# Performance work log

Measured on AMD Instinct MI355X. Metric: run time of the kernel, lower is better.

The kernel has to match this reference:

```python
import jax, jax.numpy as jnp
import numpy as np

N = 8192
IN_FEATS = 512
OUT_FEATS = 256
NEG_SLOPE = 0.01  # torch nn.LeakyReLU default


def setup_inputs() -> dict:
    key = jax.random.key(0)
    k_adj, k_feat, k_w, k_b, k_a1, k_a2 = jax.random.split(key, 6)
    adj_matrix = jax.random.uniform(k_adj, (N, N), dtype=jnp.float32)
    eye_matrix = jnp.eye(N, dtype=jnp.float32)  # identity adjacency, per AAGNN usage
    subgraph_feats = jax.random.normal(k_feat, (N, IN_FEATS), dtype=jnp.float32)
    node_mask = jnp.ones((N,), dtype=bool)
    # nn.Linear(in_feats, out_feats) params (kaiming-uniform-ish init scale)
    lim = 1.0 / np.sqrt(IN_FEATS)
    W = jax.random.uniform(k_w, (OUT_FEATS, IN_FEATS), minval=-lim, maxval=lim, dtype=jnp.float32)
    b = jax.random.uniform(k_b, (OUT_FEATS,), minval=-lim, maxval=lim, dtype=jnp.float32)
    # a_1, a_2 ~ torch.rand(1, out_feats)
    a_1 = jax.random.uniform(k_a1, (1, OUT_FEATS), dtype=jnp.float32)
    a_2 = jax.random.uniform(k_a2, (1, OUT_FEATS), dtype=jnp.float32)
    return {"adj_matrix": adj_matrix, "eye_matrix": eye_matrix,
            "subgraph_feats": subgraph_feats, "node_mask": node_mask,
            "W": W, "b": b, "a_1": a_1, "a_2": a_2}


def reference(adj_matrix, eye_matrix, subgraph_feats, node_mask, W, b, a_1, a_2):
    # z = Linear(subgraph_feats)  -> [N, out]
    z = subgraph_feats @ W.T + b
    zi = jnp.sum(a_1 * z, axis=1, keepdims=True)  # [N,1]
    zj = jnp.sum(a_2 * z, axis=1, keepdims=True)  # [N,1]
    # masked attention scores: adj*zi + adj*(eye*zj), leakyrelu, row softmax
    scores = jax.nn.leaky_relu(adj_matrix * zi + adj_matrix * (eye_matrix * zj),
                               negative_slope=NEG_SLOPE)
    att = jax.nn.softmax(scores, axis=1)  # [N,N]
    h = z - att @ z  # [N, out]
    out = jax.nn.relu(h)
    # original returns relu(h[node_mask]); mask is all-True -> same rows, static shape
    return jnp.where(node_mask[:, None], out, 0.0)
```

## Files before the change

### kernel.cpp

```cpp
#include <hip/hip_runtime.h>

#define N_NODES 8192
#define IN_F 512
#define OUT_F 256
#define KSPLIT 4
#define KCHUNK (N_NODES / KSPLIT)

typedef float f32x4 __attribute__((ext_vector_type(4)));
typedef short short8 __attribute__((ext_vector_type(8)));
typedef short short4v __attribute__((ext_vector_type(4)));

__device__ __forceinline__ unsigned short f2bf(float f) {
  unsigned int u = __float_as_uint(f);
  return (unsigned short)((u + 0x8000u) >> 16);
}

__device__ __forceinline__ short8 pack8(const float4& a, const float4& b) {
  short8 r;
  r[0] = (short)f2bf(a.x); r[1] = (short)f2bf(a.y);
  r[2] = (short)f2bf(a.z); r[3] = (short)f2bf(a.w);
  r[4] = (short)f2bf(b.x); r[5] = (short)f2bf(b.y);
  r[6] = (short)f2bf(b.z); r[7] = (short)f2bf(b.w);
  return r;
}

__global__ __launch_bounds__(256) void zgemm_mfma(
    const float* __restrict__ feats, const float* __restrict__ W,
    const float* __restrict__ bias, float* __restrict__ z,
    unsigned short* __restrict__ zT) {
  const int tid = threadIdx.x;
  const int w = tid >> 6;
  const int l = tid & 63;
  const int l4 = l >> 4;
  const int lm = l & 15;
  const int ib = blockIdx.x * 32;

  f32x4 acc[2][4];
#pragma unroll
  for (int a = 0; a < 2; ++a)
#pragma unroll
    for (int b = 0; b < 4; ++b) acc[a][b] = (f32x4){0.f, 0.f, 0.f, 0.f};

#pragma unroll 2
  for (int ks = 0; ks < 16; ++ks) {
    const int k0 = ks * 32 + l4 * 8;
    short8 afr[2], bfr[4];
#pragma unroll
    for (int it = 0; it < 2; ++it) {
      const float* p = &feats[(size_t)(ib + it * 16 + lm) * IN_F + k0];
      afr[it] = pack8(*(const float4*)p, *(const float4*)(p + 4));
    }
#pragma unroll
    for (int nt = 0; nt < 4; ++nt) {
      const float* p = &W[(size_t)(w * 64 + nt * 16 + lm) * IN_F + k0];
      bfr[nt] = pack8(*(const float4*)p, *(const float4*)(p + 4));
    }
#pragma unroll
    for (int it = 0; it < 2; ++it)
#pragma unroll
      for (int nt = 0; nt < 4; ++nt)
        acc[it][nt] = __builtin_amdgcn_mfma_f32_16x16x32_bf16(
            afr[it], bfr[nt], acc[it][nt], 0, 0, 0);
  }

#pragma unroll
  for (int nt = 0; nt < 4; ++nt) {
    const int col = w * 64 + nt * 16 + lm;
    const float bv = bias[col];
#pragma unroll
    for (int it = 0; it < 2; ++it)
#pragma unroll
      for (int r = 0; r < 4; ++r) {
        const int row = ib + it * 16 + l4 * 4 + r;
        const float v = acc[it][nt][r] + bv;
        z[(size_t)row * OUT_F + col] = v;
        zT[(size_t)col * N_NODES + row] = f2bf(v);
      }
  }
}

__global__ void zizj_kernel(const float* __restrict__ z,
                            const float* __restrict__ a1v,
                            const float* __restrict__ a2v,
                            float* __restrict__ zi, float* __restrict__ zj) {
  const int w = threadIdx.x >> 6;
  const int l = threadIdx.x & 63;
  const int row = blockIdx.x * 4 + w;
  const float4 zv = *(const float4*)&z[(size_t)row * OUT_F + l * 4];
  const float4 A1 = *(const float4*)&a1v[l * 4];
  const float4 A2 = *(const float4*)&a2v[l * 4];
  float si = zv.x * A1.x + zv.y * A1.y + zv.z * A1.z + zv.w * A1.w;
  float sj = zv.x * A2.x + zv.y * A2.y + zv.z * A2.z + zv.w * A2.w;
#pragma unroll
  for (int off = 32; off > 0; off >>= 1) {
    si += __shfl_xor(si, off);
    sj += __shfl_xor(sj, off);
  }
  if (l == 0) {
    zi[row] = si;
    zj[row] = sj;
  }
}

__global__ __launch_bounds__(256) void p_kernel(
    const float* __restrict__ adj, const float* __restrict__ zi_in,
    const float* __restrict__ zj_in, unsigned short* __restrict__ Pn) {
  __shared__ float red[4];
  const int row = blockIdx.x;
  const int tid = threadIdx.x;
  const float zir = zi_in[row];
  const float zjr = zj_in[row];
  const float* rp = adj + (size_t)row * N_NODES + tid * 4;

  f32x4 a[8];
#pragma unroll
  for (int c = 0; c < 8; ++c)
    a[c] = __builtin_nontemporal_load((const f32x4*)(rp + c * 1024));

  float psum = 0.f;
#pragma unroll
  for (int c = 0; c < 8; ++c)
#pragma unroll
    for (int e = 0; e < 4; ++e) {
      const int j = c * 1024 + tid * 4 + e;
      const float av = a[c][e];
      float s = av * zir;
      if (j == row) s += av * zjr;
      s = fmaxf(s, 0.01f * s);
      psum += __expf(s);
    }
#pragma unroll
  for (int off = 32; off > 0; off >>= 1) psum += __shfl_xor(psum, off);
  if ((tid & 63) == 0) red[tid >> 6] = psum;
  __syncthreads();
  const float rinv = 1.f / (red[0] + red[1] + red[2] + red[3]);

  unsigned short* op = Pn + (size_t)row * N_NODES + tid * 4;
#pragma unroll
  for (int c = 0; c < 8; ++c) {
    short4v v;
#pragma unroll
    for (int e = 0; e < 4; ++e) {
      const int j = c * 1024 + tid * 4 + e;
      const float av = a[c][e];
      float s = av * zir;
      if (j == row) s += av * zjr;
      s = fmaxf(s, 0.01f * s);
      v[e] = (short)f2bf(__expf(s) * rinv);
    }
    *(short4v*)(op + c * 1024) = v;
  }
}

__global__ __launch_bounds__(256) void pz_gemm(
    const unsigned short* __restrict__ Pn,
    const unsigned short* __restrict__ zT, float* __restrict__ acc_ws) {
  __shared__ __align__(16) unsigned short Pt[2][64][64];
  __shared__ __align__(16) unsigned short Zt[2][256][64];
  const int tid = threadIdx.x;
  const int w = tid >> 6;
  const int l = tid & 63;
  const int l4 = l >> 4;
  const int lm = l & 15;
  const int mt = blockIdx.x & 127;
  const int kc = blockIdx.x >> 7;
  const int ib = mt * 64;
  const int jb0 = kc * KCHUNK;

  f32x4 acc[4][4];
#pragma unroll
  for (int a = 0; a < 4; ++a)
#pragma unroll
    for (int b = 0; b < 4; ++b) acc[a][b] = (f32x4){0.f, 0.f, 0.f, 0.f};

  const int NST = KCHUNK / 64;

  {
    const int jb = jb0;
#pragma unroll
    for (int m = 0; m < 2; ++m) {
      const int g = m * 256 + tid, r = g >> 3, s = g & 7;
      *(short8*)&Pt[0][r][(s ^ (r & 7)) * 8] =
          *(const short8*)&Pn[(size_t)(ib + r) * N_NODES + jb + s * 8];
    }
#pragma unroll
    for (int m = 0; m < 8; ++m) {
      const int g = m * 256 + tid, r = g >> 3, s = g & 7;
      *(short8*)&Zt[0][r][(s ^ (r & 7)) * 8] =
          *(const short8*)&zT[(size_t)r * N_NODES + jb + s * 8];
    }
  }

  for (int st = 0; st < NST; ++st) {
    const int b = st & 1;
    __syncthreads();

    short8 pg[2], zg[8];
    if (st + 1 < NST) {
      const int jb = jb0 + (st + 1) * 64;
#pragma unroll
      for (int m = 0; m < 2; ++m) {
        const int g = m * 256 + tid, r = g >> 3, s = g & 7;
        pg[m] = *(const short8*)&Pn[(size_t)(ib + r) * N_NODES + jb + s * 8];
      }
#pragma unroll
      for (int m = 0; m < 8; ++m) {
        const int g = m * 256 + tid, r = g >> 3, s = g & 7;
        zg[m] = *(const short8*)&zT[(size_t)r * N_NODES + jb + s * 8];
      }
    }

    short8 afr[4][2], bfr[2][4];
#pragma unroll
    for (int it = 0; it < 4; ++it) {
      const int r = it * 16 + lm;
#pragma unroll
      for (int kk = 0; kk < 2; ++kk)
        afr[it][kk] = *(const short8*)&Pt[b][r][((kk * 4 + l4) ^ (r & 7)) * 8];
    }
#pragma unroll
    for (int nt = 0; nt < 4; ++nt) {
      const int r = w * 64 + nt * 16 + lm;
#pragma unroll
      for (int kk = 0; kk < 2; ++kk)
        bfr[kk][nt] = *(const short8*)&Zt[b][r][((kk * 4 + l4) ^ (r & 7)) * 8];
    }
#pragma unroll
    for (int it = 0; it < 4; ++it)
#pragma unroll
      for (int kk = 0; kk < 2; ++kk)
#pragma unroll
        for (int nt = 0; nt < 4; ++nt)
          acc[it][nt] = __builtin_amdgcn_mfma_f32_16x16x32_bf16(
              afr[it][kk], bfr[kk][nt], acc[it][nt], 0, 0, 0);

    __syncthreads();

    if (st + 1 < NST) {
#pragma unroll
      for (int m = 0; m < 2; ++m) {
        const int g = m * 256 + tid, r = g >> 3, s = g & 7;
        *(short8*)&Pt[b ^ 1][r][(s ^ (r & 7)) * 8] = pg[m];
      }
#pragma unroll
      for (int m = 0; m < 8; ++m) {
        const int g = m * 256 + tid, r = g >> 3, s = g & 7;
        *(short8*)&Zt[b ^ 1][r][(s ^ (r & 7)) * 8] = zg[m];
      }
    }
  }

#pragma unroll
  for (int it = 0; it < 4; ++it)
#pragma unroll
    for (int nt = 0; nt < 4; ++nt)
#pragma unroll
      for (int r = 0; r < 4; ++r) {
        const int gi = ib + it * 16 + l4 * 4 + r;
        const int gn = w * 64 + nt * 16 + lm;
        acc_ws[((size_t)kc * N_NODES + gi) * OUT_F + gn] = acc[it][nt][r];
      }
}

__global__ void finalize_kernel(const float* __restrict__ z,
                                const float* __restrict__ acc_ws,
                                float* __restrict__ out) {
  const int i = blockIdx.x;
  const int n = threadIdx.x;
  float a = 0.f;
#pragma unroll
  for (int kc = 0; kc < KSPLIT; ++kc)
    a += acc_ws[((size_t)kc * N_NODES + i) * OUT_F + n];
  const float v = z[(size_t)i * OUT_F + n] - a;
  out[(size_t)i * OUT_F + n] = fmaxf(v, 0.f);
}

extern "C" void kernel_launch(void* const* d_in, const int* in_sizes, int n_in,
                              void* d_out, int out_size, void* d_ws,
                              size_t ws_size, hipStream_t stream) {
  (void)in_sizes; (void)n_in; (void)out_size; (void)ws_size;
  const float* adj = (const float*)d_in[0];
  const float* feats = (const float*)d_in[2];
  const float* W = (const float*)d_in[4];
  const float* bias = (const float*)d_in[5];
  const float* a1v = (const float*)d_in[6];
  const float* a2v = (const float*)d_in[7];
  float* out = (float*)d_out;

  char* ws = (char*)d_ws;
  float* z = (float*)ws;
  unsigned short* zT = (unsigned short*)(ws + ((size_t)8 << 20));
  float* zi = (float*)(ws + ((size_t)12 << 20));
  float* zj = zi + N_NODES;
  float* acc_ws = (float*)(ws + ((size_t)16 << 20));
  unsigned short* Pn = (unsigned short*)(ws + ((size_t)96 << 20));

  hipLaunchKernelGGL(zgemm_mfma, dim3(N_NODES / 32), dim3(256), 0, stream,
                     feats, W, bias, z, zT);
  hipLaunchKernelGGL(zizj_kernel, dim3(N_NODES / 4), dim3(256), 0, stream, z,
                     a1v, a2v, zi, zj);
  hipLaunchKernelGGL(p_kernel, dim3(N_NODES), dim3(256), 0, stream, adj, zi,
                     zj, Pn);
  hipLaunchKernelGGL(pz_gemm, dim3(128 * KSPLIT), dim3(256), 0, stream, Pn,
                     zT, acc_ws);
  hipLaunchKernelGGL(finalize_kernel, dim3(N_NODES), dim3(256), 0, stream, z,
                     acc_ws, out);
}
```

Measured before the change: 160.4 us.

## Stage pz_gemm tiles with direct global-to-LDS loads and cache exp values

The pz_gemm double-buffer pipeline now uses global_load_lds to copy P and zT tiles straight into shared memory, with the XOR swizzle moved into the per-lane global address. This removes the register staging and the separate LDS write phase, and leaves one barrier per stage. Launch bounds request two blocks per CU. In p_kernel the exp values are kept in registers from the sum pass, so the second pass no longer recomputes leaky-relu and exp. The risks are higher register pressure and whether the async LDS loads are fully complete at the single barrier.

Measured after the change: 162.1 us. Within noise of the previous version (+1.1%).

```diff
diff --git a/kernel.cpp b/kernel.cpp
--- a/kernel.cpp
+++ b/kernel.cpp
@@ -22,6 +22,13 @@
   r[4] = (short)f2bf(b.x); r[5] = (short)f2bf(b.y);
   r[6] = (short)f2bf(b.z); r[7] = (short)f2bf(b.w);
   return r;
+}
+
+__device__ __forceinline__ void gload_lds16(const unsigned short* g,
+                                            unsigned short* l) {
+  __builtin_amdgcn_global_load_lds(
+      (const __attribute__((address_space(1))) unsigned int*)g,
+      (__attribute__((address_space(3))) unsigned int*)l, 16, 0, 0);
 }
 
 __global__ __launch_bounds__(256) void zgemm_mfma(
@@ -117,6 +124,7 @@
   for (int c = 0; c < 8; ++c)
     a[c] = __builtin_nontemporal_load((const f32x4*)(rp + c * 1024));
 
+  float p[32];
   float psum = 0.f;
 #pragma unroll
   for (int c = 0; c < 8; ++c)
@@ -127,8 +135,13 @@
       float s = av * zir;
       if (j == row) s += av * zjr;
       s = fmaxf(s, 0.01f * s);
-      psum += __expf(s);
-    }
+      const float pe = __expf(s);
+      p[c * 4 + e] = pe;
+      psum += pe;
+    }
+#pragma unroll
+  for (int i = 0; i < 32; ++i) asm volatile("" : "+v"(p[i]));
+
 #pragma unroll
   for (int off = 32; off > 0; off >>= 1) psum += __shfl_xor(psum, off);
   if ((tid & 63) == 0) red[tid >> 6] = psum;
@@ -140,19 +153,12 @@
   for (int c = 0; c < 8; ++c) {
     short4v v;
 #pragma unroll
-    for (int e = 0; e < 4; ++e) {
-      const int j = c * 1024 + tid * 4 + e;
-      const float av = a[c][e];
-      float s = av * zir;
-      if (j == row) s += av * zjr;
-      s = fmaxf(s, 0.01f * s);
-      v[e] = (short)f2bf(__expf(s) * rinv);
-    }
+    for (int e = 0; e < 4; ++e) v[e] = (short)f2bf(p[c * 4 + e] * rinv);
     *(short4v*)(op + c * 1024) = v;
   }
 }
 
-__global__ __launch_bounds__(256) void pz_gemm(
+__global__ __launch_bounds__(256, 2) void pz_gemm(
     const unsigned short* __restrict__ Pn,
     const unsigned short* __restrict__ zT, float* __restrict__ acc_ws) {
   __shared__ __align__(16) unsigned short Pt[2][64][64];
@@ -167,6 +173,9 @@
   const int ib = mt * 64;
   const int jb0 = kc * KCHUNK;
 
+  const int rsub = w * 8 + (l >> 3);
+  const int csw = ((l & 7) ^ (l >> 3)) * 8;
+
   f32x4 acc[4][4];
 #pragma unroll
   for (int a = 0; a < 4; ++a)
@@ -175,40 +184,24 @@
 
   const int NST = KCHUNK / 64;
 
-  {
-    const int jb = jb0;
-#pragma unroll
-    for (int m = 0; m < 2; ++m) {
-      const int g = m * 256 + tid, r = g >> 3, s = g & 7;
-      *(short8*)&Pt[0][r][(s ^ (r & 7)) * 8] =
-          *(const short8*)&Pn[(size_t)(ib + r) * N_NODES + jb + s * 8];
-    }
-#pragma unroll
-    for (int m = 0; m < 8; ++m) {
-      const int g = m * 256 + tid, r = g >> 3, s = g & 7;
-      *(short8*)&Zt[0][r][(s ^ (r & 7)) * 8] =
-          *(const short8*)&zT[(size_t)r * N_NODES + jb + s * 8];
-    }
-  }
+#define STAGE(buf, jb)                                                       \
+  {                                                                          \
+    _Pragma("unroll") for (int m = 0; m < 2; ++m) {                          \
+      gload_lds16(&Pn[(size_t)(ib + m * 32 + rsub) * N_NODES + (jb) + csw],  \
+                  &Pt[buf][0][0] + (m * 256 + w * 64) * 8);                  \
+    }                                                                        \
+    _Pragma("unroll") for (int m = 0; m < 8; ++m) {                          \
+      gload_lds16(&zT[(size_t)(m * 32 + rsub) * N_NODES + (jb) + csw],       \
+                  &Zt[buf][0][0] + (m * 256 + w * 64) * 8);                  \
+    }                                                                        \
+  }
+
+  STAGE(0, jb0);
+  __syncthreads();
 
   for (int st = 0; st < NST; ++st) {
     const int b = st & 1;
-    __syncthreads();
-
-    short8 pg[2], zg[8];
-    if (st + 1 < NST) {
-      const int jb = jb0 + (st + 1) * 64;
-#pragma unroll
-      for (int m = 0; m < 2; ++m) {
-        const int g = m * 256 + tid, r = g >> 3, s = g & 7;
-        pg[m] = *(const short8*)&Pn[(size_t)(ib + r) * N_NODES + jb + s * 8];
-      }
-#pragma unroll
-      for (int m = 0; m < 8; ++m) {
-        const int g = m * 256 + tid, r = g >> 3, s = g & 7;
-        zg[m] = *(const short8*)&zT[(size_t)r * N_NODES + jb + s * 8];
-      }
-    }
+    if (st + 1 < NST) STAGE(b ^ 1, jb0 + (st + 1) * 64);
 
     short8 afr[4][2], bfr[2][4];
 #pragma unroll
@@ -235,19 +228,6 @@
               afr[it][kk], bfr[kk][nt], acc[it][nt], 0, 0, 0);
 
     __syncthreads();
-
-    if (st + 1 < NST) {
-#pragma unroll
-      for (int m = 0; m < 2; ++m) {
-        const int g = m * 256 + tid, r = g >> 3, s = g & 7;
-        *(short8*)&Pt[b ^ 1][r][(s ^ (r & 7)) * 8] = pg[m];
-      }
-#pragma unroll
-      for (int m = 0; m < 8; ++m) {
-        const int g = m * 256 + tid, r = g >> 3, s = g & 7;
-        *(short8*)&Zt[b ^ 1][r][(s ^ (r & 7)) * 8] = zg[m];
-      }
-    }
   }
 
 #pragma unroll
```

## Load z operand directly from global, cache exp values, raise K-split

Applied to the files above, without the earlier changes.

The PZ GEMM stops staging the z tile in shared memory and has each wave read its MFMA B fragments straight from global memory, relying on L2 since all row blocks share zT. This cuts LDS use so more blocks can be resident, with a launch-bounds occupancy hint of 3. The K-split rises from 4 to 8 for more parallelism, at the cost of a larger partial-sum workspace that the finalize step must reduce. The softmax kernel keeps the 32 exponentials in registers instead of recomputing them in the second pass, which trades more registers for fewer exp evaluations.

After: 190.1 us. +18.6%, slower.

```diff
diff --git a/kernel.cpp b/kernel.cpp
--- a/kernel.cpp
+++ b/kernel.cpp
@@ -3,7 +3,7 @@
 #define N_NODES 8192
 #define IN_F 512
 #define OUT_F 256
-#define KSPLIT 4
+#define KSPLIT 8
 #define KCHUNK (N_NODES / KSPLIT)
 
 typedef float f32x4 __attribute__((ext_vector_type(4)));
@@ -117,6 +117,7 @@
   for (int c = 0; c < 8; ++c)
     a[c] = __builtin_nontemporal_load((const f32x4*)(rp + c * 1024));
 
+  float p[32];
   float psum = 0.f;
 #pragma unroll
   for (int c = 0; c < 8; ++c)
@@ -127,8 +128,13 @@
       float s = av * zir;
       if (j == row) s += av * zjr;
       s = fmaxf(s, 0.01f * s);
-      psum += __expf(s);
-    }
+      const float pe = __expf(s);
+      p[c * 4 + e] = pe;
+      psum += pe;
+    }
+#pragma unroll
+  for (int i = 0; i < 32; ++i) asm volatile("" : "+v"(p[i]));
+
 #pragma unroll
   for (int off = 32; off > 0; off >>= 1) psum += __shfl_xor(psum, off);
   if ((tid & 63) == 0) red[tid >> 6] = psum;
@@ -140,23 +146,15 @@
   for (int c = 0; c < 8; ++c) {
     short4v v;
 #pragma unroll
-    for (int e = 0; e < 4; ++e) {
-      const int j = c * 1024 + tid * 4 + e;
-      const float av = a[c][e];
-      float s = av * zir;
-      if (j == row) s += av * zjr;
-      s = fmaxf(s, 0.01f * s);
-      v[e] = (short)f2bf(__expf(s) * rinv);
-    }
+    for (int e = 0; e < 4; ++e) v[e] = (short)f2bf(p[c * 4 + e] * rinv);
     *(short4v*)(op + c * 1024) = v;
   }
 }
 
-__global__ __launch_bounds__(256) void pz_gemm(
+__global__ __launch_bounds__(256, 3) void pz_gemm(
     const unsigned short* __restrict__ Pn,
     const unsigned short* __restrict__ zT, float* __restrict__ acc_ws) {
   __shared__ __align__(16) unsigned short Pt[2][64][64];
-  __shared__ __align__(16) unsigned short Zt[2][256][64];
   const int tid = threadIdx.x;
   const int w = tid >> 6;
   const int l = tid & 63;
@@ -176,18 +174,11 @@
   const int NST = KCHUNK / 64;
 
   {
-    const int jb = jb0;
 #pragma unroll
     for (int m = 0; m < 2; ++m) {
       const int g = m * 256 + tid, r = g >> 3, s = g & 7;
       *(short8*)&Pt[0][r][(s ^ (r & 7)) * 8] =
-          *(const short8*)&Pn[(size_t)(ib + r) * N_NODES + jb + s * 8];
-    }
-#pragma unroll
-    for (int m = 0; m < 8; ++m) {
-      const int g = m * 256 + tid, r = g >> 3, s = g & 7;
-      *(short8*)&Zt[0][r][(s ^ (r & 7)) * 8] =
-          *(const short8*)&zT[(size_t)r * N_NODES + jb + s * 8];
+          *(const short8*)&Pn[(size_t)(ib + r) * N_NODES + jb0 + s * 8];
     }
   }
 
@@ -195,7 +186,7 @@
     const int b = st & 1;
     __syncthreads();
 
-    short8 pg[2], zg[8];
+    short8 pg[2];
     if (st + 1 < NST) {
       const int jb = jb0 + (st + 1) * 64;
 #pragma unroll
@@ -203,13 +194,9 @@
         const int g = m * 256 + tid, r = g >> 3, s = g & 7;
         pg[m] = *(const short8*)&Pn[(size_t)(ib + r) * N_NODES + jb + s * 8];
       }
-#pragma unroll
-      for (int m = 0; m < 8; ++m) {
-        const int g = m * 256 + tid, r = g >> 3, s = g & 7;
-        zg[m] = *(const short8*)&zT[(size_t)r * N_NODES + jb + s * 8];
-      }
-    }
-
+    }
+
+    const int jb = jb0 + st * 64;
     short8 afr[4][2], bfr[2][4];
 #pragma unroll
     for (int it = 0; it < 4; ++it) {
@@ -219,12 +206,12 @@
         afr[it][kk] = *(const short8*)&Pt[b][r][((kk * 4 + l4) ^ (r & 7)) * 8];
     }
 #pragma unroll
-    for (int nt = 0; nt < 4; ++nt) {
-      const int r = w * 64 + nt * 16 + lm;
-#pragma unroll
-      for (int kk = 0; kk < 2; ++kk)
-        bfr[kk][nt] = *(const short8*)&Zt[b][r][((kk * 4 + l4) ^ (r & 7)) * 8];
-    }
+    for (int kk = 0; kk < 2; ++kk)
+#pragma unroll
+      for (int nt = 0; nt < 4; ++nt)
+        bfr[kk][nt] =
+            *(const short8*)&zT[(size_t)(w * 64 + nt * 16 + lm) * N_NODES +
+                                jb + kk * 32 + l4 * 8];
 #pragma unroll
     for (int it = 0; it < 4; ++it)
 #pragma unroll
@@ -241,11 +228,6 @@
       for (int m = 0; m < 2; ++m) {
         const int g = m * 256 + tid, r = g >> 3, s = g & 7;
         *(short8*)&Pt[b ^ 1][r][(s ^ (r & 7)) * 8] = pg[m];
-      }
-#pragma unroll
-      for (int m = 0; m < 8; ++m) {
-        const int g = m * 256 + tid, r = g >> 3, s = g & 7;
-        *(short8*)&Zt[b ^ 1][r][(s ^ (r & 7)) * 8] = zg[m];
       }
     }
   }
```
